# Kernel optimization log

Hardware: AMD Instinct MI355X
Metric: run time of the kernel (lower is better)

Reference implementation:

```python
import jax, jax.numpy as jnp
import numpy as np

N = 100000   # nodes
G = 256      # graphs
E = 120000   # edges per relation
IN = 162
HID = 128
R = 5
L = 2        # extra RGCN layers beyond the initial one


def setup_inputs() -> dict:
    key = jax.random.key(0)
    ks = jax.random.split(key, 24)
    s = 0.05
    inp = {
        "X": jax.random.normal(ks[0], (N, IN), jnp.float32),
        "batch": jnp.sort(jax.random.randint(ks[6], (N,), 0, G)),
    }
    for i in range(R):
        inp[f"edge_index{i+1}"] = jax.random.randint(ks[1 + i], (2, E), 0, N)
    # RGCN initial layer params
    inp["W0"] = jax.random.normal(ks[7], (R, IN, HID), jnp.float32) * s
    inp["root0"] = jax.random.normal(ks[8], (IN, HID), jnp.float32) * s
    inp["b0"] = jnp.zeros((HID,), jnp.float32)
    # stacked params for the L hidden RGCN layers
    inp["Wl"] = jax.random.normal(ks[9], (L, R, HID, HID), jnp.float32) * s
    inp["rootl"] = jax.random.normal(ks[10], (L, HID, HID), jnp.float32) * s
    inp["bl"] = jnp.zeros((L, HID), jnp.float32)
    # classification head
    inp["Wc1"] = jax.random.normal(ks[11], (HID, HID), jnp.float32) * s
    inp["bc1"] = jnp.zeros((HID,), jnp.float32)
    inp["Wc2"] = jax.random.normal(ks[12], (HID, HID), jnp.float32) * s
    inp["bc2"] = jnp.zeros((HID,), jnp.float32)
    inp["Wc3"] = jax.random.normal(ks[13], (HID, 1), jnp.float32) * s
    inp["bc3"] = jnp.zeros((1,), jnp.float32)
    return inp


def _seg_mean(msg, dst, num):
    # scatter-mean over destination nodes (PyG RGCNConv uses aggr='mean' per relation)
    s = jax.ops.segment_sum(msg, dst, num_segments=num)
    c = jax.ops.segment_sum(jnp.ones(msg.shape[0], msg.dtype), dst, num_segments=num)
    return s / jnp.maximum(c, 1.0)[:, None]


def _rgcn(x, W, root, b, src, dst):
    # src, dst: [R, E]; W: [R, d_in, d_out]
    msgs = jnp.einsum("ref,rfh->reh", x[src], W)          # [R, E, HID]
    agg = jax.vmap(_seg_mean, in_axes=(0, 0, None))(msgs, dst, N)  # [R, N, HID]
    return x @ root + b + agg.sum(0)


def reference(X, edge_index1, edge_index2, edge_index3, edge_index4, edge_index5,
              batch, W0, root0, b0, Wl, rootl, bl, Wc1, bc1, Wc2, bc2, Wc3, bc3):
    ei = jnp.stack([edge_index1, edge_index2, edge_index3, edge_index4, edge_index5])  # [R,2,E]
    src, dst = ei[:, 0, :], ei[:, 1, :]
    h = jax.nn.relu(_rgcn(X, W0, root0, b0, src, dst))
    for l in range(L):
        h = jax.nn.relu(_rgcn(h, Wl[l], rootl[l], bl[l], src, dst))
    # mean readout over graphs
    s = jax.ops.segment_sum(h, batch, num_segments=G)
    c = jax.ops.segment_sum(jnp.ones((N,), h.dtype), batch, num_segments=G)
    read = s / jnp.maximum(c, 1.0)[:, None]
    h = jax.nn.relu(read @ Wc1 + bc1)
    h = jax.nn.relu(h @ Wc2 + bc2)
    return h @ Wc3 + bc3
```

## Files before the change

kernel.cpp:

```cpp
#include <hip/hip_runtime.h>

#define N_NODES 100000
#define NPAD    100096
#define NTILES  782
#define G_GRAPHS 256
#define IN_F 162
#define HID 128
#define R_REL 5
#define L_LAYERS 2
#define M5 (R_REL * N_NODES)
#define KSEG0 192
#define KC0   (6 * KSEG0)
#define KC1   (6 * HID)

typedef __attribute__((ext_vector_type(8))) short bf16x8;
typedef __attribute__((ext_vector_type(4))) float f32x4;

__device__ __forceinline__ short f2bf(float f) {
    union { float f; unsigned u; } v; v.f = f;
    unsigned r = (v.u + 0x7fffu + ((v.u >> 16) & 1u)) >> 16;
    return (short)r;
}
__device__ __forceinline__ float bf2f(unsigned short u) {
    union { unsigned u; float f; } v; v.u = ((unsigned)u) << 16;
    return v.f;
}

__global__ void k_count(const int* e0, const int* e1, const int* e2,
                        const int* e3, const int* e4, int* cnt, int E) {
    int gid = blockIdx.x * 256 + threadIdx.x;
    if (gid >= R_REL * E) return;
    int r = gid / E, e = gid - r * E;
    const int* ei = (r == 0) ? e0 : (r == 1) ? e1 : (r == 2) ? e2 : (r == 3) ? e3 : e4;
    atomicAdd(&cnt[r * N_NODES + ei[E + e]], 1);
}

__global__ __launch_bounds__(256) void k_scan1(const int* __restrict__ cnt,
                                               int* __restrict__ off, int* __restrict__ bsum) {
    __shared__ int ts[256];
    int t = threadIdx.x;
    int base = blockIdx.x * 1024 + t * 4;
    int v[4];
    #pragma unroll
    for (int j = 0; j < 4; j++) v[j] = (base + j < M5) ? cnt[base + j] : 0;
    int tsum = v[0] + v[1] + v[2] + v[3];
    ts[t] = tsum; __syncthreads();
    for (int o = 1; o < 256; o <<= 1) {
        int x = (t >= o) ? ts[t - o] : 0;
        __syncthreads();
        ts[t] += x;
        __syncthreads();
    }
    if (t == 255) bsum[blockIdx.x] = ts[255];
    int run = ts[t] - tsum;
    #pragma unroll
    for (int j = 0; j < 4; j++) { if (base + j < M5) off[base + j] = run; run += v[j]; }
}

__global__ __launch_bounds__(512) void k_scan2(int* bsum, int nblk) {
    __shared__ int ts[512];
    int t = threadIdx.x;
    int v = (t < nblk) ? bsum[t] : 0;
    ts[t] = v; __syncthreads();
    for (int o = 1; o < 512; o <<= 1) {
        int x = (t >= o) ? ts[t - o] : 0;
        __syncthreads();
        ts[t] += x;
        __syncthreads();
    }
    if (t < nblk) bsum[t] = ts[t] - v;
}

__global__ void k_scan3(const int* __restrict__ off, const int* __restrict__ bsum,
                        int* __restrict__ mstart, int* __restrict__ mcur,
                        const int* __restrict__ cnt, float* __restrict__ invc) {
    int i = blockIdx.x * 256 + threadIdx.x;
    if (i >= M5) return;
    int o = off[i] + bsum[i >> 10];
    mstart[i] = o;
    mcur[i] = o;
    int c = cnt[i];
    invc[i] = 1.0f / (float)max(c, 1);
    if (i == M5 - 1) mstart[M5] = o + c;
}

__global__ void k_fill(const int* e0, const int* e1, const int* e2,
                       const int* e3, const int* e4, int* mcur,
                       int* __restrict__ mrec, int E) {
    int gid = blockIdx.x * 256 + threadIdx.x;
    if (gid >= R_REL * E) return;
    int r = gid / E, e = gid - r * E;
    const int* ei = (r == 0) ? e0 : (r == 1) ? e1 : (r == 2) ? e2 : (r == 3) ? e3 : e4;
    int src = ei[e], dst = ei[E + e];
    int pos = atomicAdd(&mcur[r * N_NODES + dst], 1);
    mrec[pos] = src;
}

__global__ void k_castX(const float* __restrict__ X, unsigned short* __restrict__ Xb) {
    int gid = blockIdx.x * 256 + threadIdx.x;
    if (gid >= NPAD * KSEG0) return;
    int row = gid / KSEG0, k = gid - row * KSEG0;
    float v = (row < N_NODES && k < IN_F) ? X[(size_t)row * IN_F + k] : 0.f;
    Xb[gid] = (unsigned short)f2bf(v);
}

__global__ void k_tw0(const float* __restrict__ root0, const float* __restrict__ W0,
                      short* __restrict__ out) {
    int gid = blockIdx.x * 256 + threadIdx.x;
    if (gid >= 128 * KC0) return;
    int col = gid / KC0;
    int kk = gid - col * KC0;
    int chunk = kk / KSEG0, k = kk - chunk * KSEG0;
    float v = 0.f;
    if (k < IN_F)
        v = (chunk == 0) ? root0[k * HID + col]
                         : W0[((size_t)(chunk - 1) * IN_F + k) * HID + col];
    out[gid] = f2bf(v);
}

__global__ void k_twl(const float* __restrict__ rootl, const float* __restrict__ Wl,
                      short* __restrict__ out) {
    int gid = blockIdx.x * 256 + threadIdx.x;
    if (gid >= L_LAYERS * 128 * KC1) return;
    int l = gid / (128 * KC1);
    int rem = gid - l * 128 * KC1;
    int col = rem / KC1;
    int kk = rem - col * KC1;
    int chunk = kk / HID, k = kk - chunk * HID;
    float v = (chunk == 0) ? rootl[((size_t)l * HID + k) * HID + col]
                           : Wl[(((size_t)l * R_REL + (chunk - 1)) * HID + k) * HID + col];
    out[gid] = f2bf(v);
}

template<int KSEG>
__global__ __launch_bounds__(256)
void gemm_fused(const unsigned short* __restrict__ A0, const short* __restrict__ Wt,
                const float* __restrict__ bias,
                const int* __restrict__ mstart, const int* __restrict__ mrec,
                const float* __restrict__ invc,
                unsigned short* __restrict__ Hout) {
    constexpr int KS = KSEG / 32;
    constexpr int KCAT = 6 * KSEG;
    constexpr int SA = (KSEG == 192) ? 184 : 136;
    constexpr int EBUF = 384;
    __shared__ short Zs[128 * SA + 16];
    __shared__ int   sMS[5 * 129];
    __shared__ float sMW[5 * 128];
    __shared__ int   sE[EBUF];

    const int row0 = blockIdx.x * 128;
    const int tid = threadIdx.x;
    const int lane = tid & 63, wv = tid >> 6;
    const int quad = lane >> 4, l16 = lane & 15;
    const int wr0 = (wv >> 1) * 64, wc0 = (wv & 1) * 64;

    for (int i = tid; i < 5 * 129; i += 256) {
        int seg = i / 129, o = i - seg * 129;
        sMS[i] = mstart[seg * N_NODES + min(row0 + o, N_NODES)];
    }
    for (int i = tid; i < 5 * 128; i += 256) {
        int seg = i >> 7, o = i & 127;
        int d = row0 + o;
        sMW[i] = (d < N_NODES) ? invc[seg * N_NODES + d] : 0.f;
    }
    if constexpr (KSEG == 192) {
        for (int i = tid; i < 128 * 16; i += 256)
            Zs[(i >> 4) * SA + 168 + (i & 15)] = 0;
        if (tid < 16) Zs[128 * SA + tid] = 0;
    }

    const unsigned short* a0p = A0 + (size_t)(row0 + wr0 + l16) * KSEG + quad * 8;
    const short* Bp = Wt + (size_t)(wc0 + l16) * KCAT + quad * 8;

    f32x4 acc[4][4];
    #pragma unroll
    for (int i = 0; i < 4; i++)
        #pragma unroll
        for (int j = 0; j < 4; j++) acc[i][j] = (f32x4){0.f, 0.f, 0.f, 0.f};

    bf16x8 ac[4], bc[4], an[4], bn[4];
    #pragma unroll
    for (int i = 0; i < 4; i++) {
        ac[i] = *(const bf16x8*)(a0p + (size_t)i * 16 * KSEG);
        bc[i] = *(const bf16x8*)(Bp + (size_t)i * 16 * KCAT);
    }
    #pragma unroll
    for (int t = 0; t < KS; t++) {
        if (t + 1 < KS) {
            #pragma unroll
            for (int i = 0; i < 4; i++) {
                an[i] = *(const bf16x8*)(a0p + (size_t)i * 16 * KSEG + (t + 1) * 32);
                bn[i] = *(const bf16x8*)(Bp + (size_t)i * 16 * KCAT + (t + 1) * 32);
            }
        }
        #pragma unroll
        for (int i = 0; i < 4; i++)
            #pragma unroll
            for (int j = 0; j < 4; j++)
                acc[i][j] = __builtin_amdgcn_mfma_f32_16x16x32_bf16(ac[i], bc[j], acc[i][j], 0, 0, 0);
        if (t + 1 < KS) {
            #pragma unroll
            for (int i = 0; i < 4; i++) { ac[i] = an[i]; bc[i] = bn[i]; }
        }
    }
    __syncthreads();

    for (int sg = 0; sg < R_REL; sg++) {
        const int tb = (1 + sg) * KS;
        #pragma unroll
        for (int j = 0; j < 4; j++)
            bc[j] = *(const bf16x8*)(Bp + (size_t)j * 16 * KCAT + tb * 32);

        const int blo = sMS[sg * 129];
        {
            int cnt = sMS[sg * 129 + 128] - blo;
            if (cnt > EBUF) cnt = EBUF;
            for (int i = tid; i < cnt; i += 256) sE[i] = mrec[blo + i];
        }
        __syncthreads();

        {
            const int mbase = sg * 129 + wv * 32;
            const int jlo = sMS[mbase];
            const int jhi = sMS[mbase + 32];
            int di = 0;
            int bnd = sMS[mbase + 1];
            float s0 = 0.f, s1 = 0.f, s2 = 0.f, s3 = 0.f;
            const int lx = (lane & 31) * 2;

            auto FLUSH = [&]() {
                float w = sMW[sg * 128 + wv * 32 + di];
                int zr = (wv * 32 + di) * SA;
                unsigned pv = (unsigned)(unsigned short)f2bf(s0 * w) |
                              ((unsigned)(unsigned short)f2bf(s1 * w) << 16);
                *(unsigned*)&Zs[zr + lane * 2] = pv;
                if constexpr (KSEG == 192) {
                    if (lane < 20) {
                        unsigned qv = (unsigned)(unsigned short)f2bf(s2 * w) |
                                      ((unsigned)(unsigned short)f2bf(s3 * w) << 16);
                        *(unsigned*)&Zs[zr + 128 + lane * 2] = qv;
                    }
                }
                s0 = 0.f; s1 = 0.f; s2 = 0.f; s3 = 0.f;
            };

            #define GLD(i, q, u) { \
                int j_ = min(jb + i, jmax); int jj_ = j_ - blo; \
                int src_ = (jj_ < EBUF) ? sE[jj_] : mrec[j_]; \
                const unsigned short* r_ = A0 + (size_t)src_ * KSEG; \
                q = *(const unsigned*)(r_ + lane * 2); \
                if constexpr (KSEG == 192) u = *(const unsigned*)(r_ + 128 + lx); }

            #define CNS(i, q, u) if (jb + i < jhi) { \
                int j_ = jb + i; \
                while (di < 32 && j_ == bnd) { \
                    FLUSH(); di++; \
                    bnd = (di < 32) ? sMS[mbase + di + 1] : 0x7fffffff; \
                } \
                s0 += bf2f((unsigned short)(q & 0xffff)); \
                s1 += bf2f((unsigned short)(q >> 16)); \
                if constexpr (KSEG == 192) { \
                    s2 += bf2f((unsigned short)(u & 0xffff)); \
                    s3 += bf2f((unsigned short)(u >> 16)); } }

            for (int jb = jlo; jb < jhi; jb += 8) {
                const int jmax = jhi - 1;
                unsigned q0, q1, q2, q3, q4, q5, q6, q7;
                unsigned u0 = 0, u1 = 0, u2 = 0, u3 = 0, u4 = 0, u5 = 0, u6 = 0, u7 = 0;
                GLD(0, q0, u0) GLD(1, q1, u1) GLD(2, q2, u2) GLD(3, q3, u3)
                GLD(4, q4, u4) GLD(5, q5, u5) GLD(6, q6, u6) GLD(7, q7, u7)
                CNS(0, q0, u0) CNS(1, q1, u1) CNS(2, q2, u2) CNS(3, q3, u3)
                CNS(4, q4, u4) CNS(5, q5, u5) CNS(6, q6, u6) CNS(7, q7, u7)
            }
            while (di < 32) { FLUSH(); di++; }
            #undef GLD
            #undef CNS
        }
        __syncthreads();

        #pragma unroll
        for (int k = 0; k < KS; k++) {
            if (k + 1 < KS) {
                #pragma unroll
                for (int j = 0; j < 4; j++)
                    bn[j] = *(const bf16x8*)(Bp + (size_t)j * 16 * KCAT + (tb + k + 1) * 32);
            }
            #pragma unroll
            for (int i = 0; i < 4; i++)
                ac[i] = *(const bf16x8*)&Zs[(wr0 + i * 16 + l16) * SA + k * 32 + quad * 8];
            #pragma unroll
            for (int i = 0; i < 4; i++)
                #pragma unroll
                for (int j = 0; j < 4; j++)
                    acc[i][j] = __builtin_amdgcn_mfma_f32_16x16x32_bf16(ac[i], bc[j], acc[i][j], 0, 0, 0);
            if (k + 1 < KS) {
                #pragma unroll
                for (int j = 0; j < 4; j++) bc[j] = bn[j];
            }
        }
        __syncthreads();
    }

    float bj[4];
    #pragma unroll
    for (int j = 0; j < 4; j++) bj[j] = bias[wc0 + j * 16 + l16];
    #pragma unroll
    for (int i = 0; i < 4; i++)
        #pragma unroll
        for (int j = 0; j < 4; j++)
            #pragma unroll
            for (int reg = 0; reg < 4; reg++)
                Zs[(wr0 + i * 16 + quad * 4 + reg) * 136 + wc0 + j * 16 + l16] =
                    f2bf(fmaxf(acc[i][j][reg] + bj[j], 0.f));
    __syncthreads();

    #pragma unroll
    for (int s = 0; s < 8; s++) {
        int row = (tid >> 4) + s * 16;
        int col = (tid & 15) * 8;
        bf16x8 v = *(const bf16x8*)&Zs[row * 136 + col];
        *(bf16x8*)&Hout[(size_t)(row0 + row) * HID + col] = v;
    }
}

__global__ __launch_bounds__(128)
void k_pool(const unsigned short* __restrict__ h, const int* __restrict__ batch,
            float* __restrict__ pooled) {
    int c = threadIdx.x;
    int start = blockIdx.x * 128;
    if (start >= N_NODES) return;
    int end = min(start + 128, N_NODES);
    int g = batch[start];
    float s = 0.f;
    for (int i = start; i < end; i++) {
        int gi = batch[i];
        if (gi != g) { atomicAdd(&pooled[g * HID + c], s); s = 0.f; g = gi; }
        s += bf2f(h[(size_t)i * HID + c]);
    }
    atomicAdd(&pooled[g * HID + c], s);
}

__device__ int lower_bound_i(const int* a, int n, int v) {
    int lo = 0, hi = n;
    while (lo < hi) {
        int mid = (lo + hi) >> 1;
        if (a[mid] < v) lo = mid + 1; else hi = mid;
    }
    return lo;
}

__global__ __launch_bounds__(128)
void k_mlp(const float* __restrict__ pooled, const int* __restrict__ batch,
           const float* __restrict__ Wc1, const float* __restrict__ bc1,
           const float* __restrict__ Wc2, const float* __restrict__ bc2,
           const float* __restrict__ Wc3, const float* __restrict__ bc3,
           float* __restrict__ out) {
    int g = blockIdx.x;
    int c = threadIdx.x;
    __shared__ int range[2];
    if (c == 0) range[0] = lower_bound_i(batch, N_NODES, g);
    if (c == 1) range[1] = lower_bound_i(batch, N_NODES, g + 1);
    __syncthreads();
    float denom = fmaxf((float)(range[1] - range[0]), 1.0f);
    __shared__ float row[HID], h1[HID], h2[HID];
    row[c] = pooled[g * HID + c] / denom;
    __syncthreads();
    float acc = bc1[c];
    for (int k = 0; k < HID; k++) acc += row[k] * Wc1[k * HID + c];
    h1[c] = fmaxf(acc, 0.f);
    __syncthreads();
    acc = bc2[c];
    for (int k = 0; k < HID; k++) acc += h1[k] * Wc2[k * HID + c];
    h2[c] = fmaxf(acc, 0.f);
    __syncthreads();
    float t = h2[c] * Wc3[c];
    for (int off = 32; off > 0; off >>= 1) t += __shfl_down(t, off, 64);
    __shared__ float part[2];
    if ((c & 63) == 0) part[c >> 6] = t;
    __syncthreads();
    if (c == 0) out[g] = part[0] + part[1] + bc3[0];
}

extern "C" void kernel_launch(void* const* d_in, const int* in_sizes, int n_in,
                              void* d_out, int out_size, void* d_ws, size_t ws_size,
                              hipStream_t stream) {
    const float* X     = (const float*)d_in[0];
    const int*   batch = (const int*)d_in[1];
    const int*   e0 = (const int*)d_in[2];
    const int*   e1 = (const int*)d_in[3];
    const int*   e2 = (const int*)d_in[4];
    const int*   e3 = (const int*)d_in[5];
    const int*   e4 = (const int*)d_in[6];
    const float* W0    = (const float*)d_in[7];
    const float* root0 = (const float*)d_in[8];
    const float* b0    = (const float*)d_in[9];
    const float* Wl    = (const float*)d_in[10];
    const float* rootl = (const float*)d_in[11];
    const float* bl    = (const float*)d_in[12];
    const float* Wc1   = (const float*)d_in[13];
    const float* bc1   = (const float*)d_in[14];
    const float* Wc2   = (const float*)d_in[15];
    const float* bc2   = (const float*)d_in[16];
    const float* Wc3   = (const float*)d_in[17];
    const float* bc3   = (const float*)d_in[18];
    const int E = in_sizes[2] / 2;
    const int NE = R_REL * E;

    char* base = (char*)d_ws;
    size_t o = 0;
    auto carve = [&](size_t bytes) -> char* {
        char* p = base + o;
        o = (o + bytes + 255) & ~(size_t)255;
        return p;
    };
    unsigned short* h1 = (unsigned short*)carve((size_t)NPAD * HID * 2);
    unsigned short* Xb = (unsigned short*)carve((size_t)NPAD * KSEG0 * 2);
    int*   cnt    = (int*)carve((size_t)M5 * 4);
    float* invc   = (float*)carve((size_t)M5 * 4);
    int*   offsc  = (int*)carve((size_t)M5 * 4);
    int*   mstart = (int*)carve((size_t)(M5 + 1) * 4);
    int*   mrec   = (int*)carve((size_t)NE * 4);
    int*   bsum   = (int*)carve(2048);
    float* pooled = (float*)carve((size_t)G_GRAPHS * HID * 4);
    short* Wt0    = (short*)carve((size_t)128 * KC0 * 2);
    short* Wtl    = (short*)carve((size_t)L_LAYERS * 128 * KC1 * 2);
    int*   mcur   = offsc;
    unsigned short* h2 = Xb;

    hipMemsetAsync(cnt, 0, (size_t)M5 * 4, stream);
    hipMemsetAsync(pooled, 0, (size_t)G_GRAPHS * HID * 4, stream);
    int eg = (NE + 255) / 256;
    k_count<<<eg, 256, 0, stream>>>(e0, e1, e2, e3, e4, cnt, E);
    int nblk = (M5 + 1023) / 1024;
    k_scan1<<<nblk, 256, 0, stream>>>(cnt, offsc, bsum);
    k_scan2<<<1, 512, 0, stream>>>(bsum, nblk);
    k_scan3<<<(M5 + 255) / 256, 256, 0, stream>>>(offsc, bsum, mstart, mcur, cnt, invc);
    k_fill<<<eg, 256, 0, stream>>>(e0, e1, e2, e3, e4, mcur, mrec, E);
    k_castX<<<(NPAD * KSEG0 + 255) / 256, 256, 0, stream>>>(X, Xb);
    k_tw0<<<(128 * KC0 + 255) / 256, 256, 0, stream>>>(root0, W0, Wt0);
    k_twl<<<(L_LAYERS * 128 * KC1 + 255) / 256, 256, 0, stream>>>(rootl, Wl, Wtl);

    gemm_fused<KSEG0><<<NTILES, 256, 0, stream>>>(Xb, Wt0, b0, mstart, mrec, invc, h1);
    gemm_fused<HID><<<NTILES, 256, 0, stream>>>(h1, Wtl, bl, mstart, mrec, invc, h2);
    gemm_fused<HID><<<NTILES, 256, 0, stream>>>(h2, Wtl + (size_t)128 * KC1, bl + HID,
                                                mstart, mrec, invc, h1);

    k_pool<<<(N_NODES + 127) / 128, 128, 0, stream>>>(h1, batch, pooled);
    k_mlp<<<G_GRAPHS, 128, 0, stream>>>(pooled, batch, Wc1, bc1, Wc2, bc2, Wc3, bc3, (float*)d_out);
}
```

Before: 726.9 us.

## Double waves per GEMM tile and double-buffer edge-index prefetch

The fused RGCN GEMM/aggregation kernel moves from 256 to 512 threads per block. Each of the 8 waves now owns 32 output rows and gathers neighbours for 16 destination rows, so more irregular gather loads are in flight per tile. The per-relation edge-index staging buffer is double-buffered: the next relation's indices are prefetched while the current one is gathered, which removes one block barrier per relation. The layer-0 shared-memory row stride is narrowed and the explicit zero-padding of the unused columns is dropped, relying on zero-padded weights for columns beyond the real features. The cost is less MFMA work per wave and more register and scheduling pressure from the 512-thread launch bound.

```diff
diff --git a/kernel.cpp b/kernel.cpp
--- a/kernel.cpp
+++ b/kernel.cpp
@@ -133,7 +133,7 @@
 }
 
 template<int KSEG>
-__global__ __launch_bounds__(256)
+__global__ __launch_bounds__(512)
 void gemm_fused(const unsigned short* __restrict__ A0, const short* __restrict__ Wt,
                 const float* __restrict__ bias,
                 const int* __restrict__ mstart, const int* __restrict__ mrec,
@@ -141,96 +141,103 @@
                 unsigned short* __restrict__ Hout) {
     constexpr int KS = KSEG / 32;
     constexpr int KCAT = 6 * KSEG;
-    constexpr int SA = (KSEG == 192) ? 184 : 136;
+    constexpr int SA = (KSEG == 192) ? 168 : 136;
     constexpr int EBUF = 384;
-    __shared__ short Zs[128 * SA + 16];
+    __shared__ short Zs[128 * SA + 32];
     __shared__ int   sMS[5 * 129];
     __shared__ float sMW[5 * 128];
-    __shared__ int   sE[EBUF];
+    __shared__ int   sE[2][EBUF];
 
     const int row0 = blockIdx.x * 128;
     const int tid = threadIdx.x;
     const int lane = tid & 63, wv = tid >> 6;
     const int quad = lane >> 4, l16 = lane & 15;
-    const int wr0 = (wv >> 1) * 64, wc0 = (wv & 1) * 64;
-
-    for (int i = tid; i < 5 * 129; i += 256) {
+    const int wr0 = (wv >> 1) * 32, wc0 = (wv & 1) * 64;
+
+    for (int i = tid; i < 5 * 129; i += 512) {
         int seg = i / 129, o = i - seg * 129;
         sMS[i] = mstart[seg * N_NODES + min(row0 + o, N_NODES)];
     }
-    for (int i = tid; i < 5 * 128; i += 256) {
+    for (int i = tid; i < 5 * 128; i += 512) {
         int seg = i >> 7, o = i & 127;
         int d = row0 + o;
         sMW[i] = (d < N_NODES) ? invc[seg * N_NODES + d] : 0.f;
     }
-    if constexpr (KSEG == 192) {
-        for (int i = tid; i < 128 * 16; i += 256)
-            Zs[(i >> 4) * SA + 168 + (i & 15)] = 0;
-        if (tid < 16) Zs[128 * SA + tid] = 0;
-    }
+    {
+        int b0_ = mstart[min(row0, N_NODES)];
+        int c0_ = mstart[min(row0 + 128, N_NODES)] - b0_;
+        if (c0_ > EBUF) c0_ = EBUF;
+        for (int i = tid; i < c0_; i += 512) sE[0][i] = mrec[b0_ + i];
+    }
+    if (tid < 32) Zs[128 * SA + tid] = 0;
 
     const unsigned short* a0p = A0 + (size_t)(row0 + wr0 + l16) * KSEG + quad * 8;
     const short* Bp = Wt + (size_t)(wc0 + l16) * KCAT + quad * 8;
 
-    f32x4 acc[4][4];
-    #pragma unroll
-    for (int i = 0; i < 4; i++)
+    f32x4 acc[2][4];
+    #pragma unroll
+    for (int i = 0; i < 2; i++)
         #pragma unroll
         for (int j = 0; j < 4; j++) acc[i][j] = (f32x4){0.f, 0.f, 0.f, 0.f};
 
-    bf16x8 ac[4], bc[4], an[4], bn[4];
-    #pragma unroll
-    for (int i = 0; i < 4; i++) {
-        ac[i] = *(const bf16x8*)(a0p + (size_t)i * 16 * KSEG);
-        bc[i] = *(const bf16x8*)(Bp + (size_t)i * 16 * KCAT);
-    }
+    bf16x8 ac[2], bc[4], an[2], bn[4];
+    #pragma unroll
+    for (int i = 0; i < 2; i++) ac[i] = *(const bf16x8*)(a0p + (size_t)i * 16 * KSEG);
+    #pragma unroll
+    for (int j = 0; j < 4; j++) bc[j] = *(const bf16x8*)(Bp + (size_t)j * 16 * KCAT);
     #pragma unroll
     for (int t = 0; t < KS; t++) {
         if (t + 1 < KS) {
             #pragma unroll
-            for (int i = 0; i < 4; i++) {
+            for (int i = 0; i < 2; i++)
                 an[i] = *(const bf16x8*)(a0p + (size_t)i * 16 * KSEG + (t + 1) * 32);
-                bn[i] = *(const bf16x8*)(Bp + (size_t)i * 16 * KCAT + (t + 1) * 32);
-            }
+            #pragma unroll
+            for (int j = 0; j < 4; j++)
+                bn[j] = *(const bf16x8*)(Bp + (size_t)j * 16 * KCAT + (t + 1) * 32);
         }
         #pragma unroll
-        for (int i = 0; i < 4; i++)
+        for (int i = 0; i < 2; i++)
             #pragma unroll
             for (int j = 0; j < 4; j++)
                 acc[i][j] = __builtin_amdgcn_mfma_f32_16x16x32_bf16(ac[i], bc[j], acc[i][j], 0, 0, 0);
         if (t + 1 < KS) {
             #pragma unroll
-            for (int i = 0; i < 4; i++) { ac[i] = an[i]; bc[i] = bn[i]; }
+            for (int i = 0; i < 2; i++) ac[i] = an[i];
+            #pragma unroll
+            for (int j = 0; j < 4; j++) bc[j] = bn[j];
         }
     }
     __syncthreads();
 
+    int cur = 0;
     for (int sg = 0; sg < R_REL; sg++) {
         const int tb = (1 + sg) * KS;
         #pragma unroll
         for (int j = 0; j < 4; j++)
             bc[j] = *(const bf16x8*)(Bp + (size_t)j * 16 * KCAT + tb * 32);
 
-        const int blo = sMS[sg * 129];
+        if (sg + 1 < R_REL) {
+            int bn_ = sMS[(sg + 1) * 129];
+            int cn_ = sMS[(sg + 1) * 129 + 128] - bn_;
+            if (cn_ > EBUF) cn_ = EBUF;
+            int* sEn = sE[cur ^ 1];
+            for (int i = tid; i < cn_; i += 512) sEn[i] = mrec[bn_ + i];
+        }
+
         {
-            int cnt = sMS[sg * 129 + 128] - blo;
-            if (cnt > EBUF) cnt = EBUF;
-            for (int i = tid; i < cnt; i += 256) sE[i] = mrec[blo + i];
-        }
-        __syncthreads();
-
-        {
-            const int mbase = sg * 129 + wv * 32;
+            const int mbase = sg * 129 + wv * 16;
+            const int blo = sMS[sg * 129];
             const int jlo = sMS[mbase];
-            const int jhi = sMS[mbase + 32];
+            const int jhi = sMS[mbase + 16];
+            const int* sEc = sE[cur];
             int di = 0;
             int bnd = sMS[mbase + 1];
             float s0 = 0.f, s1 = 0.f, s2 = 0.f, s3 = 0.f;
             const int lx = (lane & 31) * 2;
 
             auto FLUSH = [&]() {
-                float w = sMW[sg * 128 + wv * 32 + di];
-                int zr = (wv * 32 + di) * SA;
+                float w = sMW[sg * 128 + wv * 16 + di];
+                int zr = (wv * 16 + di) * SA;
                 unsigned pv = (unsigned)(unsigned short)f2bf(s0 * w) |
                               ((unsigned)(unsigned short)f2bf(s1 * w) << 16);
                 *(unsigned*)&Zs[zr + lane * 2] = pv;
@@ -246,16 +253,16 @@
 
             #define GLD(i, q, u) { \
                 int j_ = min(jb + i, jmax); int jj_ = j_ - blo; \
-                int src_ = (jj_ < EBUF) ? sE[jj_] : mrec[j_]; \
+                int src_ = (jj_ < EBUF) ? sEc[jj_] : mrec[j_]; \
                 const unsigned short* r_ = A0 + (size_t)src_ * KSEG; \
                 q = *(const unsigned*)(r_ + lane * 2); \
                 if constexpr (KSEG == 192) u = *(const unsigned*)(r_ + 128 + lx); }
 
             #define CNS(i, q, u) if (jb + i < jhi) { \
                 int j_ = jb + i; \
-                while (di < 32 && j_ == bnd) { \
+                while (di < 16 && j_ == bnd) { \
                     FLUSH(); di++; \
-                    bnd = (di < 32) ? sMS[mbase + di + 1] : 0x7fffffff; \
+                    bnd = (di < 16) ? sMS[mbase + di + 1] : 0x7fffffff; \
                 } \
                 s0 += bf2f((unsigned short)(q & 0xffff)); \
                 s1 += bf2f((unsigned short)(q >> 16)); \
@@ -272,7 +279,7 @@
                 CNS(0, q0, u0) CNS(1, q1, u1) CNS(2, q2, u2) CNS(3, q3, u3)
                 CNS(4, q4, u4) CNS(5, q5, u5) CNS(6, q6, u6) CNS(7, q7, u7)
             }
-            while (di < 32) { FLUSH(); di++; }
+            while (di < 16) { FLUSH(); di++; }
             #undef GLD
             #undef CNS
         }
@@ -286,10 +293,10 @@
                     bn[j] = *(const bf16x8*)(Bp + (size_t)j * 16 * KCAT + (tb + k + 1) * 32);
             }
             #pragma unroll
-            for (int i = 0; i < 4; i++)
+            for (int i = 0; i < 2; i++)
                 ac[i] = *(const bf16x8*)&Zs[(wr0 + i * 16 + l16) * SA + k * 32 + quad * 8];
             #pragma unroll
-            for (int i = 0; i < 4; i++)
+            for (int i = 0; i < 2; i++)
                 #pragma unroll
                 for (int j = 0; j < 4; j++)
                     acc[i][j] = __builtin_amdgcn_mfma_f32_16x16x32_bf16(ac[i], bc[j], acc[i][j], 0, 0, 0);
@@ -299,13 +306,14 @@
             }
         }
         __syncthreads();
+        cur ^= 1;
     }
 
     float bj[4];
     #pragma unroll
     for (int j = 0; j < 4; j++) bj[j] = bias[wc0 + j * 16 + l16];
     #pragma unroll
-    for (int i = 0; i < 4; i++)
+    for (int i = 0; i < 2; i++)
         #pragma unroll
         for (int j = 0; j < 4; j++)
             #pragma unroll
@@ -315,8 +323,8 @@
     __syncthreads();
 
     #pragma unroll
-    for (int s = 0; s < 8; s++) {
-        int row = (tid >> 4) + s * 16;
+    for (int s = 0; s < 4; s++) {
+        int row = (tid >> 4) + s * 32;
         int col = (tid & 15) * 8;
         bf16x8 v = *(const bf16x8*)&Zs[row * 136 + col];
         *(bf16x8*)&Hout[(size_t)(row0 + row) * HID + col] = v;
@@ -440,9 +448,9 @@
     k_tw0<<<(128 * KC0 + 255) / 256, 256, 0, stream>>>(root0, W0, Wt0);
     k_twl<<<(L_LAYERS * 128 * KC1 + 255) / 256, 256, 0, stream>>>(rootl, Wl, Wtl);
 
-    gemm_fused<KSEG0><<<NTILES, 256, 0, stream>>>(Xb, Wt0, b0, mstart, mrec, invc, h1);
-    gemm_fused<HID><<<NTILES, 256, 0, stream>>>(h1, Wtl, bl, mstart, mrec, invc, h2);
-    gemm_fused<HID><<<NTILES, 256, 0, stream>>>(h2, Wtl + (size_t)128 * KC1, bl + HID,
+    gemm_fused<KSEG0><<<NTILES, 512, 0, stream>>>(Xb, Wt0, b0, mstart, mrec, invc, h1);
+    gemm_fused<HID><<<NTILES, 512, 0, stream>>>(h1, Wtl, bl, mstart, mrec, invc, h2);
+    gemm_fused<HID><<<NTILES, 512, 0, stream>>>(h2, Wtl + (size_t)128 * KC1, bl + HID,
                                                 mstart, mrec, invc, h1);
 
     k_pool<<<(N_NODES + 127) / 128, 128, 0, stream>>>(h1, batch, pooled);
```

Measured after the change: 810.1 us. 11.4% more time.
